# Performance work log

Measured on AMD Instinct MI355X. Metric: run time of the kernel, lower is better.

## Reference

```python
import jax, jax.numpy as jnp
import numpy as np

# YOLOv3 COCO anchors (pixels); layer_no=1 -> stride 16; masked_anchors = ALL anchors / stride
ANCHORS = np.array([[10,13],[16,30],[33,23],[30,61],[62,45],[59,119],[116,90],[156,198],[373,326]], dtype=np.float32)
STRIDE = 16.0
N_ANCHORS = 9
N_CLASSES = 80
N_CH = 5 + N_CLASSES  # 85


def setup_inputs() -> dict:
    key = jax.random.key(0)
    k1, k2, k3 = jax.random.split(key, 3)
    B, C, H, W = 16, 256, 64, 64
    xin = jax.random.normal(k1, (B, C, H, W), jnp.float32)
    conv_w = jax.random.normal(k2, (N_ANCHORS * N_CH, C), jnp.float32) * 0.02  # 1x1 conv kernel
    conv_b = jnp.zeros((N_ANCHORS * N_CH,), jnp.float32)
    prior_labels = jax.random.uniform(k3, (16, 50, 5), jnp.float32)  # [class,xc,yc,w,h] in [0,1]
    return {"xin": xin, "conv_w": conv_w, "conv_b": conv_b, "prior_labels": prior_labels}


def reference(xin, conv_w, conv_b, prior_labels):
    # Inference branch of YOLOimgLayer.forward (labels=None): decode + return pred.
    # prior_labels is consumed in the torch forward (truth_i/j indices) but unused on this path.
    B, C, H, W = xin.shape
    fsize = H
    # 1x1 conv == channel-mixing matmul
    out = jnp.einsum('bchw,oc->bohw', xin, conv_w) + conv_b[None, :, None, None]
    # (B, A, n_ch, H, W) -> (B, A, H, W, n_ch)
    out = out.reshape(B, N_ANCHORS, N_CH, fsize, fsize).transpose(0, 1, 3, 4, 2)
    # sigmoid channels [0:2] (x,y) and [4:] (obj + classes); leave w,h raw
    ch = jnp.arange(N_CH)
    sig_mask = (ch < 2) | (ch >= 4)
    out = jnp.where(sig_mask, jax.nn.sigmoid(out), out)

    anchors_g = jnp.asarray(ANCHORS / STRIDE, dtype=xin.dtype)  # (A, 2) grid units
    w_a = anchors_g[:, 0][None, :, None, None]  # broadcast over (B, A, H, W)
    h_a = anchors_g[:, 1][None, :, None, None]
    x_shift = jnp.arange(fsize, dtype=xin.dtype)[None, None, None, :]  # varies along W
    y_shift = jnp.arange(fsize, dtype=xin.dtype)[None, None, :, None]  # varies along H

    px = ((out[..., 0] - 0.5) * w_a + x_shift) * STRIDE
    py = ((out[..., 1] - 0.5) * h_a + y_shift) * STRIDE
    pw = jnp.exp(out[..., 2]) * w_a * STRIDE
    ph = jnp.exp(out[..., 3]) * h_a * STRIDE

    pred = jnp.concatenate(
        [px[..., None], py[..., None], pw[..., None], ph[..., None], out[..., 4:]], axis=-1
    )  # (B, A, H, W, 85)
    return pred
```

## Files before the change

kernel.cpp:

```cpp
#include <hip/hip_runtime.h>

typedef __attribute__((ext_vector_type(8))) short bf16x8;
typedef __attribute__((ext_vector_type(4))) float f32x4;
typedef __attribute__((ext_vector_type(4))) int i32x4;
typedef __attribute__((ext_vector_type(4))) unsigned short u16x4;

#define KDIM 256
#define HWSZ 4096
#define NOUT 765
#define NOUTP 768
#define TBYTES ((size_t)16 * NOUTP * HWSZ * 2)

__constant__ float c_AW[10] = {10.f,16.f,33.f,30.f,62.f,59.f,116.f,156.f,373.f,0.f};
__constant__ float c_AH[10] = {13.f,30.f,23.f,61.f,45.f,119.f,90.f,198.f,326.f,0.f};

__device__ __forceinline__ unsigned short f2bf(float f) {
  unsigned u = __builtin_bit_cast(unsigned, f);
  u += 0x7fffu + ((u >> 16) & 1u);
  return (unsigned short)(u >> 16);
}
__device__ __forceinline__ float bf2f(unsigned short h) {
  return __builtin_bit_cast(float, ((unsigned)h) << 16);
}
__device__ __forceinline__ float sigf(float t) {
  return 1.0f / (1.0f + __expf(-t));
}

__device__ __forceinline__ void bar_lds() {
  asm volatile("s_waitcnt lgkmcnt(0)" ::: "memory");
  __builtin_amdgcn_s_barrier();
  __builtin_amdgcn_sched_barrier(0);
}

__global__ void prep_w(const float* __restrict__ cw, unsigned short* __restrict__ wbf) {
  int e = (blockIdx.x * 256 + threadIdx.x) * 4;
  int o = e >> 8, col = e & 255;
  f32x4 v = {0.f, 0.f, 0.f, 0.f};
  if (o < NOUT) v = *reinterpret_cast<const f32x4*>(cw + o * KDIM + col);
  u16x4 u = { f2bf(v.x), f2bf(v.y), f2bf(v.z), f2bf(v.w) };
  *reinterpret_cast<u16x4*>(wbf + e) = u;
}

__global__ __launch_bounds__(512) void k1_gemm(
    const float* __restrict__ xin,
    const unsigned short* __restrict__ wbf,
    const float* __restrict__ bias,
    unsigned short* __restrict__ t)
{
  __shared__ __align__(16) unsigned short xT[64 * KDIM];

  const int b    = blockIdx.x >> 6;
  const int pc   = blockIdx.x & 63;
  const int tid  = threadIdx.x;
  const int lane = tid & 63;
  const int wv   = tid >> 6;

  {
    const float* xsrc = xin + ((size_t)b * KDIM) * HWSZ + pc * 64;
    const int p  = lane;
    const int sw = (p & 7) << 3;
    #pragma unroll
    for (int i = 0; i < 4; ++i) {
      const int c0 = (wv + 8 * i) << 3;
      float v[8];
      #pragma unroll
      for (int j = 0; j < 8; ++j) v[j] = xsrc[(size_t)(c0 + j) * HWSZ + p];
      union { i32x4 q; unsigned short us[8]; } pk;
      #pragma unroll
      for (int j = 0; j < 8; ++j) pk.us[j] = f2bf(v[j]);
      *reinterpret_cast<i32x4*>(&xT[(p << 8) + (c0 ^ sw)]) = pk.q;
    }
  }
  bar_lds();

  const int g     = lane >> 4;
  const int r16   = lane & 15;
  const int obase = wv * 96;

  f32x4 acc[6][4];
  #pragma unroll
  for (int ot = 0; ot < 6; ++ot)
    #pragma unroll
    for (int pt = 0; pt < 4; ++pt)
      acc[ot][pt] = f32x4{0.f, 0.f, 0.f, 0.f};

  const unsigned short* wptr = wbf + (unsigned)(obase + r16) * KDIM + 8 * g;
  const int sw0 = (r16 & 7) << 3;

  #pragma unroll
  for (int kk = 0; kk < 8; ++kk) {
    const int ke = (kk * 32 + 8 * g) ^ sw0;
    bf16x8 xfr[4];
    #pragma unroll
    for (int pt = 0; pt < 4; ++pt)
      xfr[pt] = __builtin_bit_cast(bf16x8,
          *reinterpret_cast<const i32x4*>(&xT[((pt * 16 + r16) << 8) + ke]));
    #pragma unroll
    for (int ot = 0; ot < 6; ++ot) {
      bf16x8 w = __builtin_bit_cast(bf16x8,
          *reinterpret_cast<const i32x4*>(wptr + ot * 16 * KDIM + kk * 32));
      #pragma unroll
      for (int pt = 0; pt < 4; ++pt)
        acc[ot][pt] = __builtin_amdgcn_mfma_f32_16x16x32_bf16(xfr[pt], w, acc[ot][pt], 0, 0, 0);
    }
  }

  #pragma unroll
  for (int ot = 0; ot < 6; ++ot) {
    const int o  = obase + ot * 16 + r16;
    const float bi = bias[o < NOUT ? o : 0];
    unsigned short* trow = t + (size_t)(b * NOUTP + o) * HWSZ + pc * 64;
    #pragma unroll
    for (int pt = 0; pt < 4; ++pt) {
      u16x4 pk = { f2bf(acc[ot][pt].x + bi), f2bf(acc[ot][pt].y + bi),
                   f2bf(acc[ot][pt].z + bi), f2bf(acc[ot][pt].w + bi) };
      *reinterpret_cast<u16x4*>(trow + pt * 16 + 4 * g) = pk;
    }
  }
}

__global__ __launch_bounds__(256) void k2_decode(
    const unsigned short* __restrict__ t,
    float* __restrict__ out)
{
  __shared__ __align__(16) float lds[128 * 85];

  const int tid   = threadIdx.x;
  const int chunk = blockIdx.x & 31;
  const int ba    = blockIdx.x >> 5;
  const int a     = ba % 9;
  const int hw0   = chunk << 7;
  const float aw  = c_AW[a], ah = c_AH[a];

  const unsigned short* tb = t + (size_t)((ba / 9) * NOUTP + a * 85) * HWSZ + hw0;

  #pragma unroll 1
  for (int e4 = tid; e4 < 2720; e4 += 256) {
    const int ch  = e4 >> 5;
    const int px0 = (e4 & 31) << 2;
    const u16x4 raw = *reinterpret_cast<const u16x4*>(tb + (size_t)ch * HWSZ + px0);
    #pragma unroll
    for (int j = 0; j < 4; ++j) {
      const float v  = bf2f(raw[j]);
      const int   hw = hw0 + px0 + j;
      float val;
      if (ch >= 4)      val = sigf(v);
      else if (ch == 0) val = (sigf(v) - 0.5f) * aw + (float)(hw & 63) * 16.0f;
      else if (ch == 1) val = (sigf(v) - 0.5f) * ah + (float)(hw >> 6) * 16.0f;
      else if (ch == 2) val = __expf(v) * aw;
      else              val = __expf(v) * ah;
      lds[(px0 + j) * 85 + ch] = val;
    }
  }
  __syncthreads();

  float* ob = out + ((size_t)ba * HWSZ + hw0) * 85;
  #pragma unroll 1
  for (int q = tid; q < 2720; q += 256)
    *reinterpret_cast<f32x4*>(ob + q * 4) = *reinterpret_cast<const f32x4*>(lds + q * 4);
}

__global__ __launch_bounds__(512) void yolo_fused(
    const float* __restrict__ xin,
    const unsigned short* __restrict__ wbf,
    const float* __restrict__ bias,
    float* __restrict__ out)
{
  __shared__ __align__(16) char smem[3 * 2720 * 4];
  unsigned short* xT  = reinterpret_cast<unsigned short*>(smem);
  float*          stg = reinterpret_cast<float*>(smem);

  const int bid  = blockIdx.x;
  const int ph   = bid & 1;
  const int pc   = (bid >> 1) & 63;
  const int b    = bid >> 7;
  const int tid  = threadIdx.x;
  const int lane = tid & 63;
  const int wv   = tid >> 6;

  {
    const int px     = tid & 31;
    const int c0base = (tid >> 5) << 3;
    const float* xsrc = xin + (size_t)b * KDIM * HWSZ + pc * 64 + ph * 32 + px;
    const int sw = (px & 7) << 3;
    #pragma unroll
    for (int i = 0; i < 2; ++i) {
      const int c0 = c0base + 128 * i;
      float v[8];
      #pragma unroll
      for (int j = 0; j < 8; ++j) v[j] = xsrc[(size_t)(c0 + j) * HWSZ];
      union { i32x4 q; unsigned short us[8]; } pk;
      #pragma unroll
      for (int j = 0; j < 8; ++j) pk.us[j] = f2bf(v[j]);
      *reinterpret_cast<i32x4*>(&xT[(px << 8) + (c0 ^ sw)]) = pk.q;
    }
  }
  bar_lds();

  const int g = lane >> 4, r16 = lane & 15, obase = wv * 96;
  f32x4 acc[6][2];
  #pragma unroll
  for (int ot = 0; ot < 6; ++ot) { acc[ot][0] = f32x4{0,0,0,0}; acc[ot][1] = f32x4{0,0,0,0}; }

  const unsigned short* wptr = wbf + (unsigned)(obase + r16) * KDIM + 8 * g;
  const int xb0 = (r16 << 8), xb1 = ((16 + r16) << 8), sw0 = (r16 & 7) << 3;

  #pragma unroll
  for (int kk = 0; kk < 8; ++kk) {
    const int ke = (kk * 32 + 8 * g) ^ sw0;
    bf16x8 x0 = __builtin_bit_cast(bf16x8, *reinterpret_cast<const i32x4*>(&xT[xb0 + ke]));
    bf16x8 x1 = __builtin_bit_cast(bf16x8, *reinterpret_cast<const i32x4*>(&xT[xb1 + ke]));
    #pragma unroll
    for (int ot = 0; ot < 6; ++ot) {
      bf16x8 w = __builtin_bit_cast(bf16x8,
          *reinterpret_cast<const i32x4*>(wptr + ot * 16 * KDIM + kk * 32));
      acc[ot][0] = __builtin_amdgcn_mfma_f32_16x16x32_bf16(x0, w, acc[ot][0], 0, 0, 0);
      acc[ot][1] = __builtin_amdgcn_mfma_f32_16x16x32_bf16(x1, w, acc[ot][1], 0, 0, 0);
    }
  }
  bar_lds();

  float bi[6];
  #pragma unroll
  for (int ot = 0; ot < 6; ++ot) {
    const int o = obase + ot * 16 + r16;
    bi[ot] = bias[o < NOUT ? o : 0];
  }
  const float ys = (float)pc * 16.0f, xs0 = (float)(ph * 32) * 16.0f;

  #pragma unroll 1
  for (int t3 = 0; t3 < 3; ++t3) {
    const int alo = 3 * t3;
    #pragma unroll
    for (int ot = 0; ot < 6; ++ot) {
      const int o = obase + ot * 16 + r16;
      const int a = o / 85;
      if (a >= alo && a < alo + 3) {
        const int ch = o - a * 85;
        const float aw = c_AW[a], ah = c_AH[a];
        float* sdst = stg + (a - alo) * 2720 + ch;
        #pragma unroll
        for (int pt = 0; pt < 2; ++pt) {
          #pragma unroll
          for (int r = 0; r < 4; ++r) {
            const int   pxl = pt * 16 + g * 4 + r;
            const float tv  = acc[ot][pt][r] + bi[ot];
            float val;
            if (ch >= 4)      val = sigf(tv);
            else if (ch == 0) val = (sigf(tv) - 0.5f) * aw + xs0 + (float)pxl * 16.0f;
            else if (ch == 1) val = (sigf(tv) - 0.5f) * ah + ys;
            else if (ch == 2) val = __expf(tv) * aw;
            else              val = __expf(tv) * ah;
            sdst[pxl * 85] = val;
          }
        }
      }
    }
    bar_lds();
    #pragma unroll 1
    for (int q = tid; q < 2040; q += 512) {
      const int al = (q >= 1360) ? 2 : (q >= 680 ? 1 : 0);
      const int a  = alo + al;
      const f32x4 v = *reinterpret_cast<const f32x4*>(stg + q * 4);
      const unsigned dstdw = ((unsigned)(b * 9 + a) * HWSZ + (unsigned)(pc * 64 + ph * 32)) * 85u
                           + (unsigned)(q - al * 680) * 4u;
      *reinterpret_cast<f32x4*>(out + dstdw) = v;
    }
    bar_lds();
  }
}

extern "C" void kernel_launch(void* const* d_in, const int* in_sizes, int n_in,
                              void* d_out, int out_size, void* d_ws, size_t ws_size,
                              hipStream_t stream) {
  const float* xin = (const float*)d_in[0];
  const float* cw  = (const float*)d_in[1];
  const float* cb  = (const float*)d_in[2];
  float* out = (float*)d_out;

  if (ws_size >= TBYTES + 393216) {
    unsigned short* t   = (unsigned short*)d_ws;
    unsigned short* wbf = (unsigned short*)((char*)d_ws + TBYTES);
    prep_w<<<dim3((NOUTP * KDIM / 4) / 256), dim3(256), 0, stream>>>(cw, wbf);
    k1_gemm<<<dim3(16 * 64), dim3(512), 0, stream>>>(xin, wbf, cb, t);
    k2_decode<<<dim3(16 * 9 * 32), dim3(256), 0, stream>>>(t, out);
  } else {
    unsigned short* wbf = (unsigned short*)d_ws;
    prep_w<<<dim3((NOUTP * KDIM / 4) / 256), dim3(256), 0, stream>>>(cw, wbf);
    yolo_fused<<<dim3(16 * 64 * 2), dim3(512), 0, stream>>>(xin, wbf, cb, out);
  }
}
```

Before: 163.6 us.

## Make GEMM blocks persistent over 32-pixel units with double-buffered LDS prefetch

The GEMM kernel now processes four 32-pixel units per block. It keeps bias in registers and prefetches the next unit's input into registers while running MFMAs on the current unit from a double-buffered LDS tile, so global load latency overlaps with compute. The decode kernel handles 64-pixel rows per block with 8-wide bf16 loads, which simplifies the grid-coordinate math and halves LDS use. The cost is fewer blocks in the GEMM (512 vs 1024) and smaller MFMA tiles per iteration, which reduces weight reuse per load.

```diff
diff --git a/kernel.cpp b/kernel.cpp
--- a/kernel.cpp
+++ b/kernel.cpp
@@ -4,11 +4,13 @@
 typedef __attribute__((ext_vector_type(4))) float f32x4;
 typedef __attribute__((ext_vector_type(4))) int i32x4;
 typedef __attribute__((ext_vector_type(4))) unsigned short u16x4;
+typedef __attribute__((ext_vector_type(8))) unsigned short u16x8;
 
 #define KDIM 256
 #define HWSZ 4096
 #define NOUT 765
 #define NOUTP 768
+#define UPB1 4
 #define TBYTES ((size_t)16 * NOUTP * HWSZ * 2)
 
 __constant__ float c_AW[10] = {10.f,16.f,33.f,30.f,62.f,59.f,116.f,156.f,373.f,0.f};
@@ -47,75 +49,105 @@
     const float* __restrict__ bias,
     unsigned short* __restrict__ t)
 {
-  __shared__ __align__(16) unsigned short xT[64 * KDIM];
-
-  const int b    = blockIdx.x >> 6;
-  const int pc   = blockIdx.x & 63;
+  __shared__ __align__(16) unsigned short xT[2][32 * 256];
+
   const int tid  = threadIdx.x;
   const int lane = tid & 63;
   const int wv   = tid >> 6;
-
-  {
-    const float* xsrc = xin + ((size_t)b * KDIM) * HWSZ + pc * 64;
-    const int p  = lane;
-    const int sw = (p & 7) << 3;
-    #pragma unroll
-    for (int i = 0; i < 4; ++i) {
-      const int c0 = (wv + 8 * i) << 3;
-      float v[8];
-      #pragma unroll
-      for (int j = 0; j < 8; ++j) v[j] = xsrc[(size_t)(c0 + j) * HWSZ + p];
-      union { i32x4 q; unsigned short us[8]; } pk;
-      #pragma unroll
-      for (int j = 0; j < 8; ++j) pk.us[j] = f2bf(v[j]);
-      *reinterpret_cast<i32x4*>(&xT[(p << 8) + (c0 ^ sw)]) = pk.q;
-    }
-  }
-  bar_lds();
-
-  const int g     = lane >> 4;
-  const int r16   = lane & 15;
+  const int g    = lane >> 4;
+  const int r16  = lane & 15;
   const int obase = wv * 96;
 
-  f32x4 acc[6][4];
-  #pragma unroll
-  for (int ot = 0; ot < 6; ++ot)
-    #pragma unroll
-    for (int pt = 0; pt < 4; ++pt)
-      acc[ot][pt] = f32x4{0.f, 0.f, 0.f, 0.f};
-
-  const unsigned short* wptr = wbf + (unsigned)(obase + r16) * KDIM + 8 * g;
-  const int sw0 = (r16 & 7) << 3;
-
-  #pragma unroll
-  for (int kk = 0; kk < 8; ++kk) {
-    const int ke = (kk * 32 + 8 * g) ^ sw0;
-    bf16x8 xfr[4];
-    #pragma unroll
-    for (int pt = 0; pt < 4; ++pt)
-      xfr[pt] = __builtin_bit_cast(bf16x8,
-          *reinterpret_cast<const i32x4*>(&xT[((pt * 16 + r16) << 8) + ke]));
-    #pragma unroll
-    for (int ot = 0; ot < 6; ++ot) {
-      bf16x8 w = __builtin_bit_cast(bf16x8,
-          *reinterpret_cast<const i32x4*>(wptr + ot * 16 * KDIM + kk * 32));
-      #pragma unroll
-      for (int pt = 0; pt < 4; ++pt)
-        acc[ot][pt] = __builtin_amdgcn_mfma_f32_16x16x32_bf16(xfr[pt], w, acc[ot][pt], 0, 0, 0);
-    }
-  }
-
+  const int u0 = blockIdx.x * UPB1;
+  const int b  = u0 >> 7;
+
+  const int spx = tid & 31;
+  const int sck = tid >> 5;
+  const int ssw = (spx & 7) << 3;
+  const int se0 = spx * 256 + ((sck * 16) ^ ssw);
+  const int se1 = spx * 256 + ((sck * 16 + 8) ^ ssw);
+  const float* xb = xin + (size_t)b * (KDIM * HWSZ);
+
+  float bi6[6];
   #pragma unroll
   for (int ot = 0; ot < 6; ++ot) {
-    const int o  = obase + ot * 16 + r16;
-    const float bi = bias[o < NOUT ? o : 0];
-    unsigned short* trow = t + (size_t)(b * NOUTP + o) * HWSZ + pc * 64;
-    #pragma unroll
-    for (int pt = 0; pt < 4; ++pt) {
-      u16x4 pk = { f2bf(acc[ot][pt].x + bi), f2bf(acc[ot][pt].y + bi),
-                   f2bf(acc[ot][pt].z + bi), f2bf(acc[ot][pt].w + bi) };
-      *reinterpret_cast<u16x4*>(trow + pt * 16 + 4 * g) = pk;
-    }
+    const int o = obase + ot * 16 + r16;
+    bi6[ot] = bias[o < NOUT ? o : 0];
+  }
+  const unsigned short* wptr = wbf + (unsigned)(obase + r16) * KDIM + 8 * g;
+  const int kxor = (r16 & 7) << 3;
+
+  {
+    const int py = (u0 >> 1) & 63, hf = u0 & 1;
+    const float* xs = xb + py * 64 + hf * 32 + spx;
+    float v[16];
+    #pragma unroll
+    for (int j = 0; j < 16; ++j) v[j] = xs[(size_t)(sck * 16 + j) * HWSZ];
+    union { i32x4 q; unsigned short us[8]; } p0, p1;
+    #pragma unroll
+    for (int j = 0; j < 8; ++j) { p0.us[j] = f2bf(v[j]); p1.us[j] = f2bf(v[8 + j]); }
+    *reinterpret_cast<i32x4*>(&xT[0][se0]) = p0.q;
+    *reinterpret_cast<i32x4*>(&xT[0][se1]) = p1.q;
+  }
+  bar_lds();
+
+  #pragma unroll 1
+  for (int i = 0; i < UPB1; ++i) {
+    const int u  = u0 + i;
+    const int py = (u >> 1) & 63, hf = u & 1;
+
+    float pf[16];
+    if (i + 1 < UPB1) {
+      const int un = u + 1;
+      const int pyn = (un >> 1) & 63, hfn = un & 1;
+      const float* xs = xb + pyn * 64 + hfn * 32 + spx;
+      #pragma unroll
+      for (int j = 0; j < 16; ++j) pf[j] = xs[(size_t)(sck * 16 + j) * HWSZ];
+    }
+
+    f32x4 acc[6][2];
+    #pragma unroll
+    for (int ot = 0; ot < 6; ++ot) {
+      acc[ot][0] = f32x4{0.f, 0.f, 0.f, 0.f};
+      acc[ot][1] = f32x4{0.f, 0.f, 0.f, 0.f};
+    }
+    const unsigned short* xbuf = &xT[i & 1][0];
+    #pragma unroll
+    for (int kk = 0; kk < 8; ++kk) {
+      const int ke = (kk * 32 + 8 * g) ^ kxor;
+      bf16x8 x0 = __builtin_bit_cast(bf16x8,
+          *reinterpret_cast<const i32x4*>(&xbuf[r16 * 256 + ke]));
+      bf16x8 x1 = __builtin_bit_cast(bf16x8,
+          *reinterpret_cast<const i32x4*>(&xbuf[(16 + r16) * 256 + ke]));
+      #pragma unroll
+      for (int ot = 0; ot < 6; ++ot) {
+        bf16x8 w = __builtin_bit_cast(bf16x8,
+            *reinterpret_cast<const i32x4*>(wptr + ot * (16 * KDIM) + kk * 32));
+        acc[ot][0] = __builtin_amdgcn_mfma_f32_16x16x32_bf16(x0, w, acc[ot][0], 0, 0, 0);
+        acc[ot][1] = __builtin_amdgcn_mfma_f32_16x16x32_bf16(x1, w, acc[ot][1], 0, 0, 0);
+      }
+    }
+
+    #pragma unroll
+    for (int ot = 0; ot < 6; ++ot) {
+      const int o = obase + ot * 16 + r16;
+      unsigned short* tr = t + (size_t)(b * NOUTP + o) * HWSZ + py * 64 + hf * 32;
+      #pragma unroll
+      for (int pt = 0; pt < 2; ++pt) {
+        u16x4 pk = { f2bf(acc[ot][pt].x + bi6[ot]), f2bf(acc[ot][pt].y + bi6[ot]),
+                     f2bf(acc[ot][pt].z + bi6[ot]), f2bf(acc[ot][pt].w + bi6[ot]) };
+        *reinterpret_cast<u16x4*>(tr + pt * 16 + 4 * g) = pk;
+      }
+    }
+
+    if (i + 1 < UPB1) {
+      union { i32x4 q; unsigned short us[8]; } p0, p1;
+      #pragma unroll
+      for (int j = 0; j < 8; ++j) { p0.us[j] = f2bf(pf[j]); p1.us[j] = f2bf(pf[8 + j]); }
+      *reinterpret_cast<i32x4*>(&xT[(i + 1) & 1][se0]) = p0.q;
+      *reinterpret_cast<i32x4*>(&xT[(i + 1) & 1][se1]) = p1.q;
+    }
+    bar_lds();
   }
 }
 
@@ -123,40 +155,41 @@
     const unsigned short* __restrict__ t,
     float* __restrict__ out)
 {
-  __shared__ __align__(16) float lds[128 * 85];
+  __shared__ __align__(16) float lds[64 * 85];
 
   const int tid   = threadIdx.x;
-  const int chunk = blockIdx.x & 31;
-  const int ba    = blockIdx.x >> 5;
+  const int chunk = blockIdx.x & 63;
+  const int ba    = blockIdx.x >> 6;
   const int a     = ba % 9;
-  const int hw0   = chunk << 7;
+  const int b9    = ba / 9;
+  const int hw0   = chunk << 6;
   const float aw  = c_AW[a], ah = c_AH[a];
-
-  const unsigned short* tb = t + (size_t)((ba / 9) * NOUTP + a * 85) * HWSZ + hw0;
+  const float yv  = (float)chunk * 16.0f;
+
+  const unsigned short* tb = t + (size_t)(b9 * NOUTP + a * 85) * HWSZ + hw0;
 
   #pragma unroll 1
-  for (int e4 = tid; e4 < 2720; e4 += 256) {
-    const int ch  = e4 >> 5;
-    const int px0 = (e4 & 31) << 2;
-    const u16x4 raw = *reinterpret_cast<const u16x4*>(tb + (size_t)ch * HWSZ + px0);
-    #pragma unroll
-    for (int j = 0; j < 4; ++j) {
-      const float v  = bf2f(raw[j]);
-      const int   hw = hw0 + px0 + j;
+  for (int e8 = tid; e8 < 680; e8 += 256) {
+    const int ch  = e8 >> 3;
+    const int px0 = (e8 & 7) << 3;
+    const u16x8 raw = *reinterpret_cast<const u16x8*>(tb + (size_t)ch * HWSZ + px0);
+    #pragma unroll
+    for (int j = 0; j < 8; ++j) {
+      const float v = bf2f(raw[j]);
       float val;
       if (ch >= 4)      val = sigf(v);
-      else if (ch == 0) val = (sigf(v) - 0.5f) * aw + (float)(hw & 63) * 16.0f;
-      else if (ch == 1) val = (sigf(v) - 0.5f) * ah + (float)(hw >> 6) * 16.0f;
+      else if (ch == 0) val = (sigf(v) - 0.5f) * aw + (float)(px0 + j) * 16.0f;
+      else if (ch == 1) val = (sigf(v) - 0.5f) * ah + yv;
       else if (ch == 2) val = __expf(v) * aw;
       else              val = __expf(v) * ah;
       lds[(px0 + j) * 85 + ch] = val;
     }
   }
-  __syncthreads();
+  bar_lds();
 
   float* ob = out + ((size_t)ba * HWSZ + hw0) * 85;
   #pragma unroll 1
-  for (int q = tid; q < 2720; q += 256)
+  for (int q = tid; q < 1360; q += 256)
     *reinterpret_cast<f32x4*>(ob + q * 4) = *reinterpret_cast<const f32x4*>(lds + q * 4);
 }
 
@@ -282,8 +315,8 @@
     unsigned short* t   = (unsigned short*)d_ws;
     unsigned short* wbf = (unsigned short*)((char*)d_ws + TBYTES);
     prep_w<<<dim3((NOUTP * KDIM / 4) / 256), dim3(256), 0, stream>>>(cw, wbf);
-    k1_gemm<<<dim3(16 * 64), dim3(512), 0, stream>>>(xin, wbf, cb, t);
-    k2_decode<<<dim3(16 * 9 * 32), dim3(256), 0, stream>>>(t, out);
+    k1_gemm<<<dim3(2048 / UPB1), dim3(512), 0, stream>>>(xin, wbf, cb, t);
+    k2_decode<<<dim3(16 * 9 * 64), dim3(256), 0, stream>>>(t, out);
   } else {
     unsigned short* wbf = (unsigned short*)d_ws;
     prep_w<<<dim3((NOUTP * KDIM / 4) / 256), dim3(256), 0, stream>>>(cw, wbf);
```

Measured after the change: 519.5 us. 218% more time.
